# Performance work log

Hardware: AMD Instinct MI355X
Metric: run time of the kernel (lower is better)

The kernel has to match this reference:

```python
import jax, jax.numpy as jnp
import numpy as np

H = 4096          # hidden_size
M = 4096          # num tokens
BLK = 128         # fp8 quant group/block size
EPS = 1e-6
FP8_MAX = 448.0   # float8_e4m3fn max


def fp8_round(x):
    # round-trip through fp8 e4m3 to emulate FP8 storage
    return x.astype(jnp.float8_e4m3fn).astype(jnp.float32)


def rms_norm(x, w, eps=EPS):
    var = jnp.mean(x * x, axis=-1, keepdims=True)
    return x * jax.lax.rsqrt(var + eps) * w


def block_fp8_linear(x, w, wscale):
    # per-token group-128 activation quant + 128x128 block-scaled fp8 GEMM
    m, k = x.shape
    kb = k // BLK
    nb = w.shape[1] // BLK
    xr = x.reshape(m, kb, BLK)
    amax = jnp.max(jnp.abs(xr), axis=-1)                      # [m, kb]
    s = jnp.maximum(amax, 1e-12) / FP8_MAX                    # group scales
    q = fp8_round(xr / s[..., None])                          # fp8 values
    xdq = (q * s[..., None]).reshape(m, k)                    # dequant acts
    # dequantize weight blockwise: w already fp8-valued floats
    wdq = (w.reshape(kb, BLK, nb, BLK) * wscale[:, None, :, None]).reshape(k, nb * BLK)
    return xdq @ wdq


def setup_inputs() -> dict:
    key = jax.random.key(0)
    ks = jax.random.split(key, 8)
    x = jax.random.normal(ks[0], (M, H), dtype=jnp.float32)
    sb = H // BLK
    d = {"x": x}
    for i in range(3):
        w = fp8_round(jax.random.uniform(ks[1 + i], (H, H), dtype=jnp.float32)).T
        d[f"w{i}"] = w
        d[f"ws{i}"] = jax.random.uniform(ks[4 + i], (sb, sb), dtype=jnp.float32)
    for i in range(4):
        d[f"nw{i}"] = jnp.ones((H,), dtype=jnp.float32)
    return d


def reference(x, w0, ws0, w1, ws1, w2, ws2, nw0, nw1, nw2, nw3):
    x = jax.nn.relu(x)
    resid = x
    y = rms_norm(x, nw0)
    x2 = block_fp8_linear(y, w0, ws0)
    resid = x2 + resid
    y2 = rms_norm(resid, nw1)
    x3 = block_fp8_linear(y2, w1, ws1)
    resid = x3 + resid
    y3 = rms_norm(resid, nw2)
    x4 = block_fp8_linear(y3, w2, ws2)
    resid = x4 + resid
    y4 = rms_norm(resid, nw3)
    return y4
```

## Files before the change

kernel.cpp:

```cpp
#include <hip/hip_runtime.h>
#include <stdint.h>

#define H 4096

typedef float v4f __attribute__((ext_vector_type(4)));
typedef long long i64;
typedef long long v2l __attribute__((ext_vector_type(2)));

__device__ __forceinline__ void gload16(const uint8_t* g, uint8_t* l) {
  __builtin_amdgcn_global_load_lds(
      (const __attribute__((address_space(1))) uint8_t*)g,
      (__attribute__((address_space(3))) uint8_t*)l, 16, 0, 0);
}

__device__ __forceinline__ int permpos(int kg) {
  const int kb = kg >> 7, b = kg & 127;
  const int ks = b >> 5, q = (b >> 3) & 3, j = b & 7;
  return kb * 128 + q * 32 + ks * 8 + j;
}

__global__ __launch_bounds__(256) void conv_w_kernel(
    const float* __restrict__ w0, const float* __restrict__ w1,
    const float* __restrict__ w2, uint8_t* __restrict__ o0,
    uint8_t* __restrict__ o1, uint8_t* __restrict__ o2) {
  const float* w = (blockIdx.z == 0) ? w0 : (blockIdx.z == 1 ? w1 : w2);
  uint8_t* o = (blockIdx.z == 0) ? o0 : (blockIdx.z == 1 ? o1 : o2);
  __shared__ __attribute__((aligned(16))) uint8_t buf[64 * 136];
  const int tid = threadIdx.x;
  const int k0 = blockIdx.y * 128, n0 = blockIdx.x * 64;
  const int n4 = tid & 15, krun = tid >> 4;

  unsigned dw[8];
#pragma unroll
  for (int i = 0; i < 8; ++i) {
    v4f f = *(const v4f*)(w + (size_t)(k0 + krun * 8 + i) * H + n0 + n4 * 4);
    unsigned p = __builtin_amdgcn_cvt_pk_fp8_f32(f.x, f.y, 0, false);
    dw[i] = __builtin_amdgcn_cvt_pk_fp8_f32(f.z, f.w, p, true);
  }
#pragma unroll
  for (int b = 0; b < 4; ++b) {
    const unsigned sel1 = 0x0c0c0000u | ((4u + b) << 8) | (unsigned)b;
    unsigned p01 = __builtin_amdgcn_perm(dw[1], dw[0], sel1);
    unsigned p23 = __builtin_amdgcn_perm(dw[3], dw[2], sel1);
    unsigned lo = __builtin_amdgcn_perm(p23, p01, 0x05040100u);
    unsigned p45 = __builtin_amdgcn_perm(dw[5], dw[4], sel1);
    unsigned p67 = __builtin_amdgcn_perm(dw[7], dw[6], sel1);
    unsigned hi = __builtin_amdgcn_perm(p67, p45, 0x05040100u);
    uint2 kk; kk.x = lo; kk.y = hi;
    *(uint2*)(buf + (n4 * 4 + b) * 136 + krun * 8) = kk;
  }
  __syncthreads();

#pragma unroll
  for (int it = 0; it < 2; ++it) {
    const int id = it * 256 + tid;
    const int n = id >> 3, c = id & 7;
    const int r0 = 8 * (c & 1) + (c >> 1);
    uint2 a = *(const uint2*)(buf + n * 136 + r0 * 8);
    uint2 b = *(const uint2*)(buf + n * 136 + (r0 + 4) * 8);
    uint4 outv; outv.x = a.x; outv.y = a.y; outv.z = b.x; outv.w = b.y;
    *(uint4*)(o + (size_t)(n0 + n) * H + k0 + c * 16) = outv;
  }
}

__global__ __launch_bounds__(256) void quant_kernel(
    const float* in, const float* __restrict__ nw, uint8_t* __restrict__ q,
    float* __restrict__ sxT, const int relu) {
  const int row = blockIdx.x, tid = threadIdx.x;
  const v4f* rp = (const v4f*)(in + (size_t)row * H) + tid * 4;
  v4f v[4];
  float ss = 0.f;
#pragma unroll
  for (int j = 0; j < 4; ++j) {
    v4f x = rp[j];
    if (relu) {
      x.x = fmaxf(x.x, 0.f); x.y = fmaxf(x.y, 0.f);
      x.z = fmaxf(x.z, 0.f); x.w = fmaxf(x.w, 0.f);
    }
    v[j] = x;
    ss += x.x * x.x + x.y * x.y + x.z * x.z + x.w * x.w;
  }
#pragma unroll
  for (int o = 32; o > 0; o >>= 1) ss += __shfl_down(ss, o);
  __shared__ float red[4];
  if ((tid & 63) == 0) red[tid >> 6] = ss;
  __syncthreads();
  ss = red[0] + red[1] + red[2] + red[3];
  const float rinv = 1.f / sqrtf(ss * (1.f / H) + 1e-6f);

  const v4f* np = ((const v4f*)nw) + tid * 4;
  v4f y[4];
  float am = 0.f;
#pragma unroll
  for (int j = 0; j < 4; ++j) {
    v4f nv = np[j];
    y[j].x = v[j].x * rinv * nv.x;
    y[j].y = v[j].y * rinv * nv.y;
    y[j].z = v[j].z * rinv * nv.z;
    y[j].w = v[j].w * rinv * nv.w;
    am = fmaxf(am, fmaxf(fmaxf(fabsf(y[j].x), fabsf(y[j].y)),
                         fmaxf(fabsf(y[j].z), fabsf(y[j].w))));
  }
#pragma unroll
  for (int o = 4; o > 0; o >>= 1) am = fmaxf(am, __shfl_xor(am, o, 8));
  const float s = fmaxf(am, 1e-12f) / 448.f;
  unsigned d[4];
#pragma unroll
  for (int j = 0; j < 4; ++j) {
    unsigned p = __builtin_amdgcn_cvt_pk_fp8_f32(y[j].x / s, y[j].y / s, 0, false);
    d[j] = __builtin_amdgcn_cvt_pk_fp8_f32(y[j].z / s, y[j].w / s, p, true);
  }
  uint8_t* base = q + (size_t)row * H + (tid >> 3) * 128;
  const int u = tid & 7;
  const int pos0 = (u >> 1) * 8 + (u & 1) * 64;
  uint2 st;
  st.x = d[0]; st.y = d[1];
  *(uint2*)(base + pos0) = st;
  st.x = d[2]; st.y = d[3];
  *(uint2*)(base + pos0 + 32) = st;
  if (u == 0) sxT[(size_t)(tid >> 3) * 4096 + row] = s;
}

__global__ __launch_bounds__(256) void norm_kernel(float* io,
                                                   const float* __restrict__ nw) {
  const int row = blockIdx.x, tid = threadIdx.x;
  v4f* rp = (v4f*)(io + (size_t)row * H);
  v4f v[4];
  float ss = 0.f;
#pragma unroll
  for (int j = 0; j < 4; ++j) {
    v4f x = rp[j * 256 + tid];
    v[j] = x;
    ss += x.x * x.x + x.y * x.y + x.z * x.z + x.w * x.w;
  }
#pragma unroll
  for (int o = 32; o > 0; o >>= 1) ss += __shfl_down(ss, o);
  __shared__ float red[4];
  if ((tid & 63) == 0) red[tid >> 6] = ss;
  __syncthreads();
  ss = red[0] + red[1] + red[2] + red[3];
  const float rinv = 1.f / sqrtf(ss * (1.f / H) + 1e-6f);
#pragma unroll
  for (int j = 0; j < 4; ++j) {
    v4f nv = ((const v4f*)nw)[j * 256 + tid];
    v4f y;
    y.x = v[j].x * rinv * nv.x;
    y.y = v[j].y * rinv * nv.y;
    y.z = v[j].z * rinv * nv.z;
    y.w = v[j].w * rinv * nv.w;
    rp[j * 256 + tid] = y;
  }
}

__global__ __launch_bounds__(256, 4) void gemm_kernel(
    const uint8_t* __restrict__ qa,
    const float* __restrict__ sxT,
    const uint8_t* __restrict__ wt,
    const float* __restrict__ ws,
    const float* resid, float* outp, const int relu) {
  __shared__ __attribute__((aligned(16))) uint8_t sA[16384];
  __shared__ __attribute__((aligned(16))) uint8_t sB[16384];
  __shared__ __attribute__((aligned(16))) float scb[128];
  __shared__ float ws_s[32];

  const int tid = threadIdx.x;
  const int n0 = blockIdx.x * 128, m0 = blockIdx.y * 128;
  if (tid < 32) ws_s[tid] = ws[tid * 32 + blockIdx.x];

  const int wv = tid >> 6, lane = tid & 63;
  const int quad = lane >> 4, l16 = lane & 15;
  const int wm = wv >> 1, wn = wv & 1;

  const int swc = (tid & 7) ^ ((tid >> 3) & 7);
  const uint8_t* gA = qa + (size_t)(m0 + (tid >> 3)) * H + swc * 16;
  const uint8_t* gB = wt + (size_t)(n0 + (tid >> 3)) * H + swc * 16;
  const uint8_t* gS = (const uint8_t*)sxT + (size_t)m0 * 4 + lane * 16;
  uint8_t* lA = sA + wv * 1024;
  uint8_t* lB = sB + wv * 1024;

  int offp[2];
#pragma unroll
  for (int ksp = 0; ksp < 2; ++ksp)
    offp[ksp] = (((quad * 2 + ksp) ^ (l16 & 7)) << 4);
  const int arow = (wm * 64 + l16) * 128;
  const int brow = (wn * 64 + l16) * 128;
  const int scoff = wm * 64 + quad * 4;

  const v4f zf = {0.f, 0.f, 0.f, 0.f};
  v4f acc[4][4];
#pragma unroll
  for (int i = 0; i < 4; ++i)
#pragma unroll
    for (int j = 0; j < 4; ++j) acc[i][j] = zf;

  for (int kb = 0; kb < 32; ++kb) {
#pragma unroll
    for (int i = 0; i < 4; ++i) {
      gload16(gA + (size_t)i * (32 * H), lA + i * 4096);
      gload16(gB + (size_t)i * (32 * H), lB + i * 4096);
    }
    if (wv == 0 && lane < 32) gload16(gS + (size_t)kb * 16384, (uint8_t*)scb);
    gA += 128;
    gB += 128;
    __syncthreads();

    const float wsk = ws_s[kb];
    v2l bf[4][2];
#pragma unroll
    for (int tc = 0; tc < 4; ++tc)
#pragma unroll
      for (int ksp = 0; ksp < 2; ++ksp)
        bf[tc][ksp] = *(const v2l*)(sB + brow + tc * 2048 + offp[ksp]);

#pragma unroll
    for (int tr = 0; tr < 4; ++tr) {
      const v2l a0 = *(const v2l*)(sA + arow + tr * 2048 + offp[0]);
      const v2l a1 = *(const v2l*)(sA + arow + tr * 2048 + offp[1]);
      const v4f s4 = *(const v4f*)(scb + scoff + tr * 16) * wsk;
#pragma unroll
      for (int tc = 0; tc < 4; ++tc) {
        v4f p = __builtin_amdgcn_mfma_f32_16x16x32_fp8_fp8(a0.x, bf[tc][0].x, zf, 0, 0, 0);
        p = __builtin_amdgcn_mfma_f32_16x16x32_fp8_fp8(a0.y, bf[tc][0].y, p, 0, 0, 0);
        p = __builtin_amdgcn_mfma_f32_16x16x32_fp8_fp8(a1.x, bf[tc][1].x, p, 0, 0, 0);
        p = __builtin_amdgcn_mfma_f32_16x16x32_fp8_fp8(a1.y, bf[tc][1].y, p, 0, 0, 0);
        acc[tr][tc] += p * s4;
      }
    }
    __syncthreads();
  }

  const int mB = m0 + wm * 64 + quad * 4;
  const int nB = n0 + wn * 64 + l16;
#pragma unroll
  for (int tr = 0; tr < 4; ++tr) {
#pragma unroll
    for (int r = 0; r < 4; ++r) {
      const size_t rowOff = (size_t)(mB + tr * 16 + r) * H;
#pragma unroll
      for (int tc = 0; tc < 4; ++tc) {
        const size_t idx = rowOff + nB + tc * 16;
        float rv = resid[idx];
        if (relu) rv = fmaxf(rv, 0.f);
        outp[idx] = acc[tr][tc][r] + rv;
      }
    }
  }
}

extern "C" void kernel_launch(void* const* d_in, const int* in_sizes, int n_in,
                              void* d_out, int out_size, void* d_ws, size_t ws_size,
                              hipStream_t stream) {
  const float* x   = (const float*)d_in[0];
  const float* w0  = (const float*)d_in[1];
  const float* ws0 = (const float*)d_in[2];
  const float* w1  = (const float*)d_in[3];
  const float* ws1 = (const float*)d_in[4];
  const float* w2  = (const float*)d_in[5];
  const float* ws2 = (const float*)d_in[6];
  const float* nw0 = (const float*)d_in[7];
  const float* nw1 = (const float*)d_in[8];
  const float* nw2 = (const float*)d_in[9];
  const float* nw3 = (const float*)d_in[10];
  float* R = (float*)d_out;

  uint8_t* base = (uint8_t*)d_ws;
  uint8_t* wq0 = base;
  uint8_t* wq1 = base + ((size_t)16 << 20);
  uint8_t* wq2 = base + ((size_t)32 << 20);
  uint8_t* qa  = base + ((size_t)48 << 20);
  float* sa    = (float*)(base + ((size_t)64 << 20));

  conv_w_kernel<<<dim3(64, 32, 3), 256, 0, stream>>>(w0, w1, w2, wq0, wq1, wq2);

  quant_kernel<<<4096, 256, 0, stream>>>(x, nw0, qa, sa, 1);
  gemm_kernel<<<dim3(32, 32), 256, 0, stream>>>(qa, sa, wq0, ws0, x, R, 1);

  quant_kernel<<<4096, 256, 0, stream>>>(R, nw1, qa, sa, 0);
  gemm_kernel<<<dim3(32, 32), 256, 0, stream>>>(qa, sa, wq1, ws1, R, R, 0);

  quant_kernel<<<4096, 256, 0, stream>>>(R, nw2, qa, sa, 0);
  gemm_kernel<<<dim3(32, 32), 256, 0, stream>>>(qa, sa, wq2, ws2, R, R, 0);

  norm_kernel<<<4096, 256, 0, stream>>>(R, nw3);
}
```

Measured before the change: 696.3 us.

## Pre-tile fp8 operands into MFMA fragment layout and load GEMM directly from global

Weights and quantized activations are now written in a tiled layout that matches the 16x16x32 MFMA fragment order, so each lane can fetch its A/B fragments with contiguous 16-byte global loads. The GEMM drops LDS staging and block barriers, double-buffering fragments in registers instead, with launch bounds relaxed to allow more registers. The quant kernel is reorganised so each thread handles one 128-wide group of a row. The aim is to remove LDS traffic and sync overhead, at the cost of heavier register use and no data reuse across waves, which increases L2/global traffic.

```diff
diff --git a/kernel.cpp b/kernel.cpp
--- a/kernel.cpp
+++ b/kernel.cpp
@@ -7,17 +7,6 @@
 typedef long long i64;
 typedef long long v2l __attribute__((ext_vector_type(2)));
 
-__device__ __forceinline__ void gload16(const uint8_t* g, uint8_t* l) {
-  __builtin_amdgcn_global_load_lds(
-      (const __attribute__((address_space(1))) uint8_t*)g,
-      (__attribute__((address_space(3))) uint8_t*)l, 16, 0, 0);
-}
-
-__device__ __forceinline__ int permpos(int kg) {
-  const int kb = kg >> 7, b = kg & 127;
-  const int ks = b >> 5, q = (b >> 3) & 3, j = b & 7;
-  return kb * 128 + q * 32 + ks * 8 + j;
-}
 
 __global__ __launch_bounds__(256) void conv_w_kernel(
     const float* __restrict__ w0, const float* __restrict__ w1,
@@ -28,6 +17,7 @@
   __shared__ __attribute__((aligned(16))) uint8_t buf[64 * 136];
   const int tid = threadIdx.x;
   const int k0 = blockIdx.y * 128, n0 = blockIdx.x * 64;
+  const int kbY = blockIdx.y;
   const int n4 = tid & 15, krun = tid >> 4;
 
   unsigned dw[8];
@@ -59,66 +49,75 @@
     uint2 a = *(const uint2*)(buf + n * 136 + r0 * 8);
     uint2 b = *(const uint2*)(buf + n * 136 + (r0 + 4) * 8);
     uint4 outv; outv.x = a.x; outv.y = a.y; outv.z = b.x; outv.w = b.y;
-    *(uint4*)(o + (size_t)(n0 + n) * H + k0 + c * 16) = outv;
-  }
-}
-
-__global__ __launch_bounds__(256) void quant_kernel(
+    const int nn = n0 + n;
+    *(uint4*)(o + (((size_t)(nn >> 4)) << 16) + (size_t)kbY * 2048 + c * 256 +
+              (nn & 15) * 16) = outv;
+  }
+}
+
+__global__ __launch_bounds__(512) void quant_kernel(
     const float* in, const float* __restrict__ nw, uint8_t* __restrict__ q,
     float* __restrict__ sxT, const int relu) {
-  const int row = blockIdx.x, tid = threadIdx.x;
-  const v4f* rp = (const v4f*)(in + (size_t)row * H) + tid * 4;
-  v4f v[4];
+  const int tid = threadIdx.x;
+  const int r = tid & 15, kb = tid >> 4;
+  const int row = blockIdx.x * 16 + r;
+  const float* rp = in + (size_t)row * H + kb * 128;
+
+  v4f v[32];
   float ss = 0.f;
 #pragma unroll
-  for (int j = 0; j < 4; ++j) {
-    v4f x = rp[j];
+  for (int i = 0; i < 32; ++i) {
+    v4f x = *(const v4f*)(rp + i * 4);
     if (relu) {
       x.x = fmaxf(x.x, 0.f); x.y = fmaxf(x.y, 0.f);
       x.z = fmaxf(x.z, 0.f); x.w = fmaxf(x.w, 0.f);
     }
-    v[j] = x;
+    v[i] = x;
     ss += x.x * x.x + x.y * x.y + x.z * x.z + x.w * x.w;
   }
-#pragma unroll
-  for (int o = 32; o > 0; o >>= 1) ss += __shfl_down(ss, o);
-  __shared__ float red[4];
-  if ((tid & 63) == 0) red[tid >> 6] = ss;
+  ss += __shfl_xor(ss, 16);
+  ss += __shfl_xor(ss, 32);
+  __shared__ float red[8][16];
+  if ((tid & 63) < 16) red[tid >> 6][tid & 15] = ss;
   __syncthreads();
-  ss = red[0] + red[1] + red[2] + red[3];
-  const float rinv = 1.f / sqrtf(ss * (1.f / H) + 1e-6f);
-
-  const v4f* np = ((const v4f*)nw) + tid * 4;
-  v4f y[4];
+  float tot = 0.f;
+#pragma unroll
+  for (int w8 = 0; w8 < 8; ++w8) tot += red[w8][r];
+  const float rinv = 1.f / sqrtf(tot * (1.f / H) + 1e-6f);
+
+  const float* np = nw + kb * 128;
   float am = 0.f;
 #pragma unroll
-  for (int j = 0; j < 4; ++j) {
-    v4f nv = np[j];
-    y[j].x = v[j].x * rinv * nv.x;
-    y[j].y = v[j].y * rinv * nv.y;
-    y[j].z = v[j].z * rinv * nv.z;
-    y[j].w = v[j].w * rinv * nv.w;
-    am = fmaxf(am, fmaxf(fmaxf(fabsf(y[j].x), fabsf(y[j].y)),
-                         fmaxf(fabsf(y[j].z), fabsf(y[j].w))));
-  }
-#pragma unroll
-  for (int o = 4; o > 0; o >>= 1) am = fmaxf(am, __shfl_xor(am, o, 8));
+  for (int i = 0; i < 32; ++i) {
+    v4f nv = *(const v4f*)(np + i * 4);
+    v4f y = v[i] * rinv * nv;
+    v[i] = y;
+    am = fmaxf(am, fmaxf(fmaxf(fabsf(y.x), fabsf(y.y)),
+                         fmaxf(fabsf(y.z), fabsf(y.w))));
+  }
   const float s = fmaxf(am, 1e-12f) / 448.f;
-  unsigned d[4];
-#pragma unroll
-  for (int j = 0; j < 4; ++j) {
-    unsigned p = __builtin_amdgcn_cvt_pk_fp8_f32(y[j].x / s, y[j].y / s, 0, false);
-    d[j] = __builtin_amdgcn_cvt_pk_fp8_f32(y[j].z / s, y[j].w / s, p, true);
-  }
-  uint8_t* base = q + (size_t)row * H + (tid >> 3) * 128;
-  const int u = tid & 7;
-  const int pos0 = (u >> 1) * 8 + (u & 1) * 64;
-  uint2 st;
-  st.x = d[0]; st.y = d[1];
-  *(uint2*)(base + pos0) = st;
-  st.x = d[2]; st.y = d[3];
-  *(uint2*)(base + pos0 + 32) = st;
-  if (u == 0) sxT[(size_t)(tid >> 3) * 4096 + row] = s;
+  unsigned dw[8][4];
+#pragma unroll
+  for (int u = 0; u < 8; ++u) {
+#pragma unroll
+    for (int k4 = 0; k4 < 4; ++k4) {
+      v4f y = v[u * 4 + k4];
+      unsigned p = __builtin_amdgcn_cvt_pk_fp8_f32(y.x / s, y.y / s, 0, false);
+      dw[u][k4] = __builtin_amdgcn_cvt_pk_fp8_f32(y.z / s, y.w / s, p, true);
+    }
+  }
+  uint8_t* qb = q + (((size_t)blockIdx.x) << 16) + kb * 2048 + r * 16;
+#pragma unroll
+  for (int c = 0; c < 8; ++c) {
+    const int ua = (c >> 2) + 4 * (c & 1);
+    const int ub = ua + 2;
+    const int vs = ((c >> 1) & 1) * 2;
+    uint4 st;
+    st.x = dw[ua][vs]; st.y = dw[ua][vs + 1];
+    st.z = dw[ub][vs]; st.w = dw[ub][vs + 1];
+    *(uint4*)(qb + c * 256) = st;
+  }
+  sxT[(size_t)kb * 4096 + row] = s;
 }
 
 __global__ __launch_bounds__(256) void norm_kernel(float* io,
@@ -152,39 +151,22 @@
   }
 }
 
-__global__ __launch_bounds__(256, 4) void gemm_kernel(
+__global__ __launch_bounds__(256, 2) void gemm_kernel(
     const uint8_t* __restrict__ qa,
     const float* __restrict__ sxT,
     const uint8_t* __restrict__ wt,
     const float* __restrict__ ws,
     const float* resid, float* outp, const int relu) {
-  __shared__ __attribute__((aligned(16))) uint8_t sA[16384];
-  __shared__ __attribute__((aligned(16))) uint8_t sB[16384];
-  __shared__ __attribute__((aligned(16))) float scb[128];
-  __shared__ float ws_s[32];
-
   const int tid = threadIdx.x;
-  const int n0 = blockIdx.x * 128, m0 = blockIdx.y * 128;
-  if (tid < 32) ws_s[tid] = ws[tid * 32 + blockIdx.x];
-
   const int wv = tid >> 6, lane = tid & 63;
   const int quad = lane >> 4, l16 = lane & 15;
   const int wm = wv >> 1, wn = wv & 1;
-
-  const int swc = (tid & 7) ^ ((tid >> 3) & 7);
-  const uint8_t* gA = qa + (size_t)(m0 + (tid >> 3)) * H + swc * 16;
-  const uint8_t* gB = wt + (size_t)(n0 + (tid >> 3)) * H + swc * 16;
-  const uint8_t* gS = (const uint8_t*)sxT + (size_t)m0 * 4 + lane * 16;
-  uint8_t* lA = sA + wv * 1024;
-  uint8_t* lB = sB + wv * 1024;
-
-  int offp[2];
-#pragma unroll
-  for (int ksp = 0; ksp < 2; ++ksp)
-    offp[ksp] = (((quad * 2 + ksp) ^ (l16 & 7)) << 4);
-  const int arow = (wm * 64 + l16) * 128;
-  const int brow = (wn * 64 + l16) * 128;
-  const int scoff = wm * 64 + quad * 4;
+  const int coff = quad * 512 + l16 * 16;
+
+  const uint8_t* Abase = qa + (((size_t)(blockIdx.y * 8 + wm * 4)) << 16) + coff;
+  const uint8_t* Bbase = wt + (((size_t)(blockIdx.x * 8 + wn * 4)) << 16) + coff;
+  const float* Sbase = sxT + blockIdx.y * 128 + wm * 64 + quad * 4;
+  const float* wsp = ws + blockIdx.x;
 
   const v4f zf = {0.f, 0.f, 0.f, 0.f};
   v4f acc[4][4];
@@ -193,44 +175,54 @@
 #pragma unroll
     for (int j = 0; j < 4; ++j) acc[i][j] = zf;
 
-  for (int kb = 0; kb < 32; ++kb) {
-#pragma unroll
-    for (int i = 0; i < 4; ++i) {
-      gload16(gA + (size_t)i * (32 * H), lA + i * 4096);
-      gload16(gB + (size_t)i * (32 * H), lB + i * 4096);
-    }
-    if (wv == 0 && lane < 32) gload16(gS + (size_t)kb * 16384, (uint8_t*)scb);
-    gA += 128;
-    gB += 128;
-    __syncthreads();
-
-    const float wsk = ws_s[kb];
-    v2l bf[4][2];
-#pragma unroll
-    for (int tc = 0; tc < 4; ++tc)
-#pragma unroll
-      for (int ksp = 0; ksp < 2; ++ksp)
-        bf[tc][ksp] = *(const v2l*)(sB + brow + tc * 2048 + offp[ksp]);
-
-#pragma unroll
-    for (int tr = 0; tr < 4; ++tr) {
-      const v2l a0 = *(const v2l*)(sA + arow + tr * 2048 + offp[0]);
-      const v2l a1 = *(const v2l*)(sA + arow + tr * 2048 + offp[1]);
-      const v4f s4 = *(const v4f*)(scb + scoff + tr * 16) * wsk;
-#pragma unroll
-      for (int tc = 0; tc < 4; ++tc) {
-        v4f p = __builtin_amdgcn_mfma_f32_16x16x32_fp8_fp8(a0.x, bf[tc][0].x, zf, 0, 0, 0);
-        p = __builtin_amdgcn_mfma_f32_16x16x32_fp8_fp8(a0.y, bf[tc][0].y, p, 0, 0, 0);
-        p = __builtin_amdgcn_mfma_f32_16x16x32_fp8_fp8(a1.x, bf[tc][1].x, p, 0, 0, 0);
-        p = __builtin_amdgcn_mfma_f32_16x16x32_fp8_fp8(a1.y, bf[tc][1].y, p, 0, 0, 0);
-        acc[tr][tc] += p * s4;
-      }
-    }
-    __syncthreads();
-  }
-
-  const int mB = m0 + wm * 64 + quad * 4;
-  const int nB = n0 + wn * 64 + l16;
+  v2l Af0[4][2], Bf0[4][2], Af1[4][2], Bf1[4][2];
+  v4f Sf0[4], Sf1[4];
+
+#define LOADSET(AF, BF, SF, KB)                                         \
+  do {                                                                  \
+    const size_t ko = (size_t)(KB) * 2048;                              \
+    const float* sp = Sbase + (size_t)(KB) * 4096;                      \
+    _Pragma("unroll") for (int t = 0; t < 4; ++t) {                     \
+      AF[t][0] = *(const v2l*)(Abase + ((size_t)t << 16) + ko);         \
+      AF[t][1] = *(const v2l*)(Abase + ((size_t)t << 16) + ko + 256);   \
+      BF[t][0] = *(const v2l*)(Bbase + ((size_t)t << 16) + ko);         \
+      BF[t][1] = *(const v2l*)(Bbase + ((size_t)t << 16) + ko + 256);   \
+      SF[t] = *(const v4f*)(sp + t * 16);                               \
+    }                                                                   \
+  } while (0)
+
+#define STEPSET(AF, BF, SF, KB)                                                        \
+  do {                                                                                 \
+    const float wsk = wsp[(KB) * 32];                                                  \
+    _Pragma("unroll") for (int tr = 0; tr < 4; ++tr) {                                 \
+      const v4f s4 = SF[tr] * wsk;                                                     \
+      _Pragma("unroll") for (int tc = 0; tc < 4; ++tc) {                               \
+        v4f p = __builtin_amdgcn_mfma_f32_16x16x32_fp8_fp8(AF[tr][0].x, BF[tc][0].x,   \
+                                                           zf, 0, 0, 0);               \
+        p = __builtin_amdgcn_mfma_f32_16x16x32_fp8_fp8(AF[tr][0].y, BF[tc][0].y, p,    \
+                                                       0, 0, 0);                       \
+        p = __builtin_amdgcn_mfma_f32_16x16x32_fp8_fp8(AF[tr][1].x, BF[tc][1].x, p,    \
+                                                       0, 0, 0);                       \
+        p = __builtin_amdgcn_mfma_f32_16x16x32_fp8_fp8(AF[tr][1].y, BF[tc][1].y, p,    \
+                                                       0, 0, 0);                       \
+        acc[tr][tc] += p * s4;                                                         \
+      }                                                                                \
+    }                                                                                  \
+  } while (0)
+
+  LOADSET(Af0, Bf0, Sf0, 0);
+#pragma unroll 1
+  for (int kb = 0; kb < 32; kb += 2) {
+    LOADSET(Af1, Bf1, Sf1, kb + 1);
+    STEPSET(Af0, Bf0, Sf0, kb);
+    if (kb + 2 < 32) LOADSET(Af0, Bf0, Sf0, kb + 2);
+    STEPSET(Af1, Bf1, Sf1, kb + 1);
+  }
+#undef LOADSET
+#undef STEPSET
+
+  const int mB = blockIdx.y * 128 + wm * 64 + quad * 4;
+  const int nB = blockIdx.x * 128 + wn * 64 + l16;
 #pragma unroll
   for (int tr = 0; tr < 4; ++tr) {
 #pragma unroll
@@ -272,13 +264,13 @@
 
   conv_w_kernel<<<dim3(64, 32, 3), 256, 0, stream>>>(w0, w1, w2, wq0, wq1, wq2);
 
-  quant_kernel<<<4096, 256, 0, stream>>>(x, nw0, qa, sa, 1);
+  quant_kernel<<<256, 512, 0, stream>>>(x, nw0, qa, sa, 1);
   gemm_kernel<<<dim3(32, 32), 256, 0, stream>>>(qa, sa, wq0, ws0, x, R, 1);
 
-  quant_kernel<<<4096, 256, 0, stream>>>(R, nw1, qa, sa, 0);
+  quant_kernel<<<256, 512, 0, stream>>>(R, nw1, qa, sa, 0);
   gemm_kernel<<<dim3(32, 32), 256, 0, stream>>>(qa, sa, wq1, ws1, R, R, 0);
 
-  quant_kernel<<<4096, 256, 0, stream>>>(R, nw2, qa, sa, 0);
+  quant_kernel<<<256, 512, 0, stream>>>(R, nw2, qa, sa, 0);
   gemm_kernel<<<dim3(32, 32), 256, 0, stream>>>(qa, sa, wq2, ws2, R, R, 0);
 
   norm_kernel<<<4096, 256, 0, stream>>>(R, nw3);
```

After: 1.686 ms. +142.2%, slower.
